# Kernel optimization log

Measured on AMD Instinct MI355X. Metric: run time of the kernel, lower is better.

The kernel has to match this reference:

```python
import jax, jax.numpy as jnp
import numpy as np

B, S, H, D = 4, 1024, 16, 128
E = H * D  # 2048
TOTAL = B * S
NUM_SLOTS = 2 * TOTAL


def setup_inputs() -> dict:
    key = jax.random.key(0)
    k1, k2, k3, k4, k5 = jax.random.split(key, 5)
    return {
        "hidden_states": jax.random.normal(k1, (TOTAL, E), dtype=jnp.float32) * 0.02,
        "c_attn_w": jax.random.normal(k2, (E, 3 * E), dtype=jnp.float32) * 0.02,
        "c_attn_b": jax.random.normal(k3, (3 * E,), dtype=jnp.float32) * 0.02,
        "c_proj_w": jax.random.normal(k4, (E, E), dtype=jnp.float32) * 0.02,
        "c_proj_b": jax.random.normal(k5, (E,), dtype=jnp.float32) * 0.02,
        "key_cache": jnp.zeros((NUM_SLOTS, H, D), dtype=jnp.float32),
        "value_cache": jnp.zeros((NUM_SLOTS, H, D), dtype=jnp.float32),
        "slots": jnp.arange(TOTAL, dtype=jnp.int32),
        "seq_len": S,
    }


def reference(hidden_states, c_attn_w, c_attn_b, c_proj_w, c_proj_b,
              key_cache, value_cache, slots, seq_len):
    total, embed = hidden_states.shape
    n_heads, head_dim = key_cache.shape[1], key_cache.shape[2]
    b = total // seq_len

    # fused QKV projection (fan_in_fan_out: y = x @ W + b)
    qkv = hidden_states @ c_attn_w + c_attn_b            # [total, 3E]
    qkv = qkv.reshape(total, 3, n_heads, head_dim)
    q, k, v = qkv[:, 0], qkv[:, 1], qkv[:, 2]

    # paged_attention.reshape_and_cache: scatter new k/v into the paged cache
    key_cache = key_cache.at[slots].set(k)
    value_cache = value_cache.at[slots].set(v)
    # prefill attention reads current tokens' k/v (gathered back from cache)
    k = key_cache[slots]
    v = value_cache[slots]

    # varlen causal flash attention over b equal-length sequences
    qb = q.reshape(b, seq_len, n_heads, head_dim)
    kb = k.reshape(b, seq_len, n_heads, head_dim)
    vb = v.reshape(b, seq_len, n_heads, head_dim)
    scale = jnp.asarray(head_dim, qb.dtype) ** -0.5       # softmax_scale
    scores = jnp.einsum("bqhd,bkhd->bhqk", qb, kb) * scale
    causal = jnp.tril(jnp.ones((seq_len, seq_len), dtype=bool))
    scores = jnp.where(causal, scores, jnp.finfo(scores.dtype).min)
    attn = jax.nn.softmax(scores, axis=-1)
    ctx = jnp.einsum("bhqk,bkhd->bqhd", attn, vb)
    ctx = ctx.reshape(total, embed)

    # output projection (fan_in_fan_out row-parallel linear)
    out = ctx @ c_proj_w + c_proj_b
    return out
```

## Files before the change

### kernel.cpp

```cpp
#include <hip/hip_runtime.h>
#include <stdint.h>

typedef __bf16 bf16x8 __attribute__((ext_vector_type(8)));
typedef float  f32x4  __attribute__((ext_vector_type(4)));

#define DEV static __device__ __forceinline__

DEV unsigned short f2bf(float x) {
    union { float f; unsigned int u; } v; v.f = x;
    unsigned int r = v.u + 0x7FFFu + ((v.u >> 16) & 1u);
    return (unsigned short)(r >> 16);
}

DEV unsigned short f2bf_hw(float x) {
    return __builtin_bit_cast(unsigned short, static_cast<__bf16>(x));
}

DEV void gl_lds16(const void* g, void* l) {
    __builtin_amdgcn_global_load_lds(
        (__attribute__((address_space(1))) void*)(g),
        (__attribute__((address_space(3))) void*)(l), 16, 0, 0);
}

DEV f32x4 zero4() { f32x4 z; z[0]=0.f; z[1]=0.f; z[2]=0.f; z[3]=0.f; return z; }

__global__ void k_prep(const float* __restrict__ hs, unsigned short* __restrict__ hs_bf,
                       const float* __restrict__ wqkv, unsigned short* __restrict__ wqkvT,
                       const float* __restrict__ wproj, unsigned short* __restrict__ wprojT) {
    __shared__ float tile[32][33];
    const int bid = blockIdx.x, t = threadIdx.x;
    if (bid < 2048) {
        #pragma unroll
        for (int j = 0; j < 4; j++) {
            int i = bid*4096 + j*1024 + t*4;
            float4 f = *(const float4*)(hs + i);
            ushort4 o;
            o.x = f2bf(f.x); o.y = f2bf(f.y); o.z = f2bf(f.z); o.w = f2bf(f.w);
            *(ushort4*)(hs_bf + i) = o;
        }
        return;
    }
    const float* in; unsigned short* out; int K, N, n0, k0;
    if (bid < 14336) {
        int ti = bid - 2048;
        in = wqkv; out = wqkvT; K = 2048; N = 6144;
        n0 = (ti % 192) * 32; k0 = (ti / 192) * 32;
    } else {
        int ti = bid - 14336;
        in = wproj; out = wprojT; K = 2048; N = 2048;
        n0 = (ti % 64) * 32; k0 = (ti / 64) * 32;
    }
    const int tr = t >> 3;
    const int tc = (t & 7) * 4;
    float4 f = *(const float4*)(in + (size_t)(k0 + tr) * N + n0 + tc);
    tile[tr][tc+0] = f.x; tile[tr][tc+1] = f.y; tile[tr][tc+2] = f.z; tile[tr][tc+3] = f.w;
    __syncthreads();
    ushort4 o;
    o.x = f2bf(tile[tc+0][tr]);
    o.y = f2bf(tile[tc+1][tr]);
    o.z = f2bf(tile[tc+2][tr]);
    o.w = f2bf(tile[tc+3][tr]);
    *(ushort4*)(out + (size_t)(n0 + tr) * K + k0 + tc) = o;
}

__launch_bounds__(256, 4)
__global__ void k_gemm_qkv(const unsigned short* __restrict__ A,
                           const unsigned short* __restrict__ BT,
                           const float* __restrict__ bias,
                           unsigned short* __restrict__ q_buf,
                           unsigned short* __restrict__ k_buf,
                           unsigned short* __restrict__ vt_buf,
                           int K) {
    __shared__ __align__(16) uint4 As[128*8];
    __shared__ __align__(16) uint4 Bs[128*8];

    const int t = threadIdx.x;
    const int wave = t >> 6, lane = t & 63, quad = lane >> 4, l15 = lane & 15;
    const int wm = wave & 1, wn = wave >> 1;
    const int bm = blockIdx.x, bn = blockIdx.y;

    f32x4 acc[4][4];
    #pragma unroll
    for (int i = 0; i < 4; i++)
        #pragma unroll
        for (int j = 0; j < 4; j++) acc[i][j] = zero4();

    int rS[4], gS[4];
    #pragma unroll
    for (int p = 0; p < 4; p++) {
        int c = p*4 + wave;
        int s = c*64 + lane;
        int r = s >> 3;
        rS[p] = r; gS[p] = (lane & 7) ^ (r & 7);
    }
    const unsigned short* Abase = A  + (size_t)(bm*128) * K;
    const unsigned short* Bbase = BT + (size_t)(bn*128) * K;

    const int kiters = K >> 6;
    for (int kk = 0; kk < kiters; kk++) {
        const int k0 = kk * 64;
        __syncthreads();
        #pragma unroll
        for (int p = 0; p < 4; p++) {
            int c = p*4 + wave;
            gl_lds16(Abase + (size_t)rS[p]*K + k0 + gS[p]*8, &As[c*64]);
            gl_lds16(Bbase + (size_t)rS[p]*K + k0 + gS[p]*8, &Bs[c*64]);
        }
        __syncthreads();
        #pragma unroll
        for (int ks = 0; ks < 2; ks++) {
            bf16x8 af[4], bfr[4];
            #pragma unroll
            for (int mt = 0; mt < 4; mt++) {
                int row = wm*64 + mt*16 + l15;
                int g = (ks*4 + quad) ^ (row & 7);
                af[mt] = __builtin_bit_cast(bf16x8, As[row*8 + g]);
            }
            #pragma unroll
            for (int nt = 0; nt < 4; nt++) {
                int row = wn*64 + nt*16 + l15;
                int g = (ks*4 + quad) ^ (row & 7);
                bfr[nt] = __builtin_bit_cast(bf16x8, Bs[row*8 + g]);
            }
            #pragma unroll
            for (int mt = 0; mt < 4; mt++)
                #pragma unroll
                for (int nt = 0; nt < 4; nt++)
                    acc[mt][nt] = __builtin_amdgcn_mfma_f32_16x16x32_bf16(
                        af[mt], bfr[nt], acc[mt][nt], 0, 0, 0);
        }
    }

    const int nglob = bn * 128;
    const int seg = nglob >> 11;
    const int cn_base = (nglob & 2047) + wn*64;
    if (seg < 2) {
        unsigned short* dst = (seg == 0) ? q_buf : k_buf;
        const float scl = (seg == 0) ? 0.12751743f : 1.0f;
        #pragma unroll
        for (int nt = 0; nt < 4; nt++) {
            int cn = cn_base + nt*16 + l15;
            float bv = bias[nglob + wn*64 + nt*16 + l15];
            #pragma unroll
            for (int mt = 0; mt < 4; mt++) {
                int tt = bm*128 + wm*64 + mt*16 + quad*4;
                #pragma unroll
                for (int r = 0; r < 4; r++)
                    dst[(size_t)(tt + r) * 2048 + cn] = f2bf((acc[mt][nt][r] + bv) * scl);
            }
        }
    } else {
        #pragma unroll
        for (int nt = 0; nt < 4; nt++) {
            int cn = cn_base + nt*16 + l15;
            int h = cn >> 7, d = cn & 127;
            float bv = bias[nglob + wn*64 + nt*16 + l15];
            #pragma unroll
            for (int mt = 0; mt < 4; mt++) {
                int tt = bm*128 + wm*64 + mt*16 + quad*4;
                int b = tt >> 10, s = tt & 1023;
                ushort4 pk;
                pk.x = f2bf(acc[mt][nt][0] + bv);
                pk.y = f2bf(acc[mt][nt][1] + bv);
                pk.z = f2bf(acc[mt][nt][2] + bv);
                pk.w = f2bf(acc[mt][nt][3] + bv);
                *(ushort4*)(vt_buf + ((size_t)((b*16 + h)*128 + d) * 1024 + s)) = pk;
            }
        }
    }
}

__launch_bounds__(256, 4)
__global__ void k_gemm_proj(const unsigned short* __restrict__ A,
                            const unsigned short* __restrict__ BT,
                            const float* __restrict__ bias,
                            float* __restrict__ outp,
                            int N, int K) {
    __shared__ __align__(16) uint4 As[128*8];
    __shared__ __align__(16) uint4 Bs[128*8];

    const int t = threadIdx.x;
    const int wave = t >> 6, lane = t & 63, quad = lane >> 4, l15 = lane & 15;
    const int wm = wave & 1, wn = wave >> 1;
    const int bm = blockIdx.x, bn = blockIdx.y;

    f32x4 acc[4][4];
    #pragma unroll
    for (int i = 0; i < 4; i++)
        #pragma unroll
        for (int j = 0; j < 4; j++) acc[i][j] = zero4();

    int rS[4], gS[4];
    #pragma unroll
    for (int p = 0; p < 4; p++) {
        int c = p*4 + wave;
        int s = c*64 + lane;
        int r = s >> 3;
        rS[p] = r; gS[p] = (lane & 7) ^ (r & 7);
    }
    const unsigned short* Abase = A  + (size_t)(bm*128) * K;
    const unsigned short* Bbase = BT + (size_t)(bn*128) * K;

    const int kiters = K >> 6;
    for (int kk = 0; kk < kiters; kk++) {
        const int k0 = kk * 64;
        __syncthreads();
        #pragma unroll
        for (int p = 0; p < 4; p++) {
            int c = p*4 + wave;
            gl_lds16(Abase + (size_t)rS[p]*K + k0 + gS[p]*8, &As[c*64]);
            gl_lds16(Bbase + (size_t)rS[p]*K + k0 + gS[p]*8, &Bs[c*64]);
        }
        __syncthreads();
        #pragma unroll
        for (int ks = 0; ks < 2; ks++) {
            bf16x8 af[4], bfr[4];
            #pragma unroll
            for (int mt = 0; mt < 4; mt++) {
                int row = wm*64 + mt*16 + l15;
                int g = (ks*4 + quad) ^ (row & 7);
                af[mt] = __builtin_bit_cast(bf16x8, As[row*8 + g]);
            }
            #pragma unroll
            for (int nt = 0; nt < 4; nt++) {
                int row = wn*64 + nt*16 + l15;
                int g = (ks*4 + quad) ^ (row & 7);
                bfr[nt] = __builtin_bit_cast(bf16x8, Bs[row*8 + g]);
            }
            #pragma unroll
            for (int mt = 0; mt < 4; mt++)
                #pragma unroll
                for (int nt = 0; nt < 4; nt++)
                    acc[mt][nt] = __builtin_amdgcn_mfma_f32_16x16x32_bf16(
                        af[mt], bfr[nt], acc[mt][nt], 0, 0, 0);
        }
    }

    #pragma unroll
    for (int nt = 0; nt < 4; nt++) {
        int n = bn*128 + wn*64 + nt*16 + l15;
        float bv = bias[n];
        #pragma unroll
        for (int mt = 0; mt < 4; mt++) {
            int m = bm*128 + wm*64 + mt*16 + quad*4;
            #pragma unroll
            for (int r = 0; r < 4; r++)
                outp[(size_t)(m + r) * N + n] = acc[mt][nt][r] + bv;
        }
    }
}

__launch_bounds__(256, 2)
__global__ void k_attn(const unsigned short* __restrict__ q_buf,
                       const unsigned short* __restrict__ k_buf,
                       const unsigned short* __restrict__ vt_buf,
                       unsigned short* __restrict__ ctx_buf) {
    extern __shared__ char smem[];
    uint4* Ks = (uint4*)smem;
    uint4* Vs = (uint4*)(smem + 32768);
    unsigned short* Pl = (unsigned short*)(smem + 65536);

    const int t = threadIdx.x;
    const int wave = t >> 6, lane = t & 63, quad = lane >> 4, l15 = lane & 15;
    const int bh = blockIdx.x;
    const int yq = blockIdx.y;
    const int qt = (yq < 4) ? yq : (11 - yq);
    const int b = bh >> 4, h = bh & 15;

    bf16x8 qf[2][4];
    #pragma unroll
    for (int rt = 0; rt < 2; rt++) {
        const size_t qoff = (size_t)(b*1024 + qt*128 + wave*32 + rt*16 + l15) * 2048 + h*128;
        #pragma unroll
        for (int ks = 0; ks < 4; ks++)
            qf[rt][ks] = __builtin_bit_cast(bf16x8, *(const uint4*)(q_buf + qoff + ks*32 + quad*8));
    }

    f32x4 ctx[2][8];
    #pragma unroll
    for (int rt = 0; rt < 2; rt++)
        #pragma unroll
        for (int i = 0; i < 8; i++) ctx[rt][i] = zero4();
    float l_run[2][4];
    #pragma unroll
    for (int rt = 0; rt < 2; rt++)
        #pragma unroll
        for (int r = 0; r < 4; r++) l_run[rt][r] = 0.f;

    const size_t kbase = (size_t)b * 1024 * 2048 + h*128;
    const size_t vbase = (size_t)(b*16 + h) * 131072;
    const int row0 = qt*128 + wave*32;
    const int kiters = 2*qt + 2;

    unsigned short* Plw = Pl + wave*1024;

    {
        #pragma unroll
        for (int p = 0; p < 4; p++) {
            int c = p*4 + wave;
            {   int s = c*64 + lane;
                int r = s >> 4;
                int g = (s & 15) ^ (r & 15);
                gl_lds16(k_buf + kbase + (size_t)(0*64 + r) * 2048 + g*8, Ks + c*64);
            }
            {   int s = c*64 + lane;
                int r = s >> 3;
                int g = (lane & 7) ^ (r & 7);
                gl_lds16(vt_buf + vbase + (size_t)r * 1024 + 0*64 + g*8, Vs + c*64);
            }
        }
    }
    __syncthreads();

    for (int kt = 0; kt < kiters; kt++) {
        const int d = kt & 1;

        if (kt + 1 < kiters) {
            const int dn = d ^ 1;
            #pragma unroll
            for (int p = 0; p < 4; p++) {
                int c = p*4 + wave;
                {   int s = c*64 + lane;
                    int r = s >> 4;
                    int g = (s & 15) ^ (r & 15);
                    gl_lds16(k_buf + kbase + (size_t)((kt+1)*64 + r) * 2048 + g*8,
                             Ks + dn*1024 + c*64);
                }
                {   int s = c*64 + lane;
                    int r = s >> 3;
                    int g = (lane & 7) ^ (r & 7);
                    gl_lds16(vt_buf + vbase + (size_t)r * 1024 + (kt+1)*64 + g*8,
                             Vs + dn*1024 + c*64);
                }
            }
        }

        if (kt*64 <= row0 + 31) {
            const bool needmask = (kt*64 + 63 > row0);
            const uint4* Kd = Ks + d*1024;
            const uint4* Vd = Vs + d*1024;

            f32x4 sacc[2][4];
            #pragma unroll
            for (int rt = 0; rt < 2; rt++)
                #pragma unroll
                for (int nt = 0; nt < 4; nt++) sacc[rt][nt] = zero4();
            #pragma unroll
            for (int ks = 0; ks < 4; ks++)
                #pragma unroll
                for (int nt = 0; nt < 4; nt++) {
                    int key = nt*16 + l15;
                    int g = (ks*4 + quad) ^ (key & 15);
                    bf16x8 kf = __builtin_bit_cast(bf16x8, Kd[key*16 + g]);
                    sacc[0][nt] = __builtin_amdgcn_mfma_f32_16x16x32_bf16(qf[0][ks], kf, sacc[0][nt], 0, 0, 0);
                    sacc[1][nt] = __builtin_amdgcn_mfma_f32_16x16x32_bf16(qf[1][ks], kf, sacc[1][nt], 0, 0, 0);
                }

            #pragma unroll
            for (int rt = 0; rt < 2; rt++) {
                float pv[4][4];
                if (needmask) {
                    #pragma unroll
                    for (int nt = 0; nt < 4; nt++)
                        #pragma unroll
                        for (int r = 0; r < 4; r++) {
                            bool masked = (kt*64 + nt*16 + l15 > row0 + rt*16 + quad*4 + r);
                            pv[nt][r] = masked ? 0.f : __builtin_amdgcn_exp2f(sacc[rt][nt][r]);
                        }
                } else {
                    #pragma unroll
                    for (int nt = 0; nt < 4; nt++)
                        #pragma unroll
                        for (int r = 0; r < 4; r++)
                            pv[nt][r] = __builtin_amdgcn_exp2f(sacc[rt][nt][r]);
                }
                #pragma unroll
                for (int r = 0; r < 4; r++)
                    l_run[rt][r] += (pv[0][r] + pv[1][r]) + (pv[2][r] + pv[3][r]);

                #pragma unroll
                for (int nt = 0; nt < 4; nt++)
                    #pragma unroll
                    for (int r = 0; r < 4; r++) {
                        int row = quad*4 + r;
                        int col = nt*16 + l15;
                        int gc = (col >> 3) ^ (row & 7);
                        Plw[row*64 + gc*8 + (col & 7)] = f2bf_hw(pv[nt][r]);
                    }
                __asm__ volatile("s_waitcnt lgkmcnt(0)" ::: "memory");

                #pragma unroll
                for (int ks = 0; ks < 2; ks++) {
                    int gp = (ks*4 + quad) ^ (l15 & 7);
                    bf16x8 pa = __builtin_bit_cast(bf16x8, *(const uint4*)&Plw[l15*64 + gp*8]);
                    #pragma unroll
                    for (int dt = 0; dt < 8; dt++) {
                        int drow = dt*16 + l15;
                        int gv = (ks*4 + quad) ^ (drow & 7);
                        bf16x8 vf = __builtin_bit_cast(bf16x8, Vd[drow*8 + gv]);
                        ctx[rt][dt] = __builtin_amdgcn_mfma_f32_16x16x32_bf16(pa, vf, ctx[rt][dt], 0, 0, 0);
                    }
                }
            }
        }

        __syncthreads();
    }

    #pragma unroll
    for (int rt = 0; rt < 2; rt++) {
        float inv[4];
        #pragma unroll
        for (int r = 0; r < 4; r++) {
            float l = l_run[rt][r];
            l += __shfl_xor(l, 1);
            l += __shfl_xor(l, 2);
            l += __shfl_xor(l, 4);
            l += __shfl_xor(l, 8);
            inv[r] = 1.0f / l;
        }
        const int tt0 = b*1024 + qt*128 + wave*32 + rt*16 + quad*4;
        #pragma unroll
        for (int dt = 0; dt < 8; dt++)
            #pragma unroll
            for (int r = 0; r < 4; r++)
                ctx_buf[(size_t)(tt0 + r) * 2048 + h*128 + dt*16 + l15] = f2bf_hw(ctx[rt][dt][r] * inv[r]);
    }
}

extern "C" void kernel_launch(void* const* d_in, const int* in_sizes, int n_in,
                              void* d_out, int out_size, void* d_ws, size_t ws_size,
                              hipStream_t stream) {
    const float* hs    = (const float*)d_in[0];
    const float* wqkv  = (const float*)d_in[1];
    const float* bqkv  = (const float*)d_in[2];
    const float* wproj = (const float*)d_in[3];
    const float* bproj = (const float*)d_in[4];

    char* ws = (char*)d_ws;
    unsigned short* hs_bf   = (unsigned short*)(ws);
    unsigned short* wqkvT   = (unsigned short*)(ws + 16777216ull);
    unsigned short* wprojT  = (unsigned short*)(ws + 41943040ull);
    unsigned short* q_buf   = (unsigned short*)(ws + 50331648ull);
    unsigned short* k_buf   = (unsigned short*)(ws + 67108864ull);
    unsigned short* vt_buf  = (unsigned short*)(ws + 83886080ull);
    unsigned short* ctx_buf = (unsigned short*)(ws + 100663296ull);

    static bool attr_set = false;
    if (!attr_set) {
        (void)hipFuncSetAttribute((const void*)k_attn,
                                  hipFuncAttributeMaxDynamicSharedMemorySize, 73728);
        attr_set = true;
    }

    k_prep<<<18432, 256, 0, stream>>>(hs, hs_bf, wqkv, wqkvT, wproj, wprojT);
    k_gemm_qkv<<<dim3(32, 48), 256, 0, stream>>>(hs_bf, wqkvT, bqkv, q_buf, k_buf, vt_buf, 2048);
    k_attn<<<dim3(64, 8), 256, 73728, stream>>>(q_buf, k_buf, vt_buf, ctx_buf);
    k_gemm_proj<<<dim3(32, 16), 256, 0, stream>>>(ctx_buf, wprojT, bproj, (float*)d_out, 2048, 2048);
}
```

Before: 381.8 us.

## Restructure QKV GEMM into 256x192 tiles with double-buffered LDS prefetch

Rewrites the QKV projection GEMM to use 512-thread workgroups computing 256x192 output tiles. The next K-slice is prefetched into a double-buffered dynamic LDS region while MFMAs run on the current one, with wave priority raised around the MFMA bursts. A swizzled block index improves L2 reuse across the 512 workgroups. The aim is to hide global-to-LDS latency and raise arithmetic intensity, at the cost of 112 KB LDS, one workgroup per CU, and higher register pressure.

```diff
diff --git a/kernel.cpp b/kernel.cpp
--- a/kernel.cpp
+++ b/kernel.cpp
@@ -63,101 +63,126 @@
     *(ushort4*)(out + (size_t)(n0 + tr) * K + k0 + tc) = o;
 }
 
-__launch_bounds__(256, 4)
+#define ST_A(NXT,K0,J) gl_lds16(Abase + (size_t)rA[J]*2048 + (K0) + gA[J], As + (NXT)*2048 + (J)*512 + dstw)
+#define ST_B(NXT,K0,J) gl_lds16(Bbase + (size_t)rB[J]*2048 + (K0) + gB[J], Bs + (NXT)*1536 + (J)*512 + dstw)
+
+#define QKV_TILE(CUR, NXT, TK)                                                  \
+  {                                                                             \
+    const uint4* Ar = As + (CUR)*2048;                                          \
+    const uint4* Br = Bs + (CUR)*1536;                                          \
+    const bool st = (TK) + 1 < 32;                                              \
+    const int kn = ((TK) + 1) * 64;                                             \
+    _Pragma("unroll")                                                           \
+    for (int p = 0; p < 4; ++p) {                                               \
+      const int mh = p >> 1, ks = p & 1;                                        \
+      bf16x8 af[4], bfr[3];                                                     \
+      _Pragma("unroll")                                                         \
+      for (int mt = 0; mt < 4; ++mt) {                                          \
+        int row = wm*128 + mh*64 + mt*16 + l15;                                 \
+        int g = (ks*4 + quad) ^ (row & 7);                                      \
+        af[mt] = __builtin_bit_cast(bf16x8, Ar[row*8 + g]);                     \
+      }                                                                         \
+      _Pragma("unroll")                                                         \
+      for (int nt = 0; nt < 3; ++nt) {                                          \
+        int row = wn*48 + nt*16 + l15;                                          \
+        int g = (ks*4 + quad) ^ (row & 7);                                      \
+        bfr[nt] = __builtin_bit_cast(bf16x8, Br[row*8 + g]);                    \
+      }                                                                         \
+      if (st && p == 0) { ST_A(NXT,kn,0); ST_A(NXT,kn,1); ST_A(NXT,kn,2); ST_A(NXT,kn,3); } \
+      if (st && p == 1) { ST_B(NXT,kn,0); ST_B(NXT,kn,1); ST_B(NXT,kn,2); }     \
+      __builtin_amdgcn_s_barrier();                                             \
+      __builtin_amdgcn_s_setprio(1);                                            \
+      _Pragma("unroll")                                                         \
+      for (int mt = 0; mt < 4; ++mt)                                            \
+        _Pragma("unroll")                                                       \
+        for (int nt = 0; nt < 3; ++nt)                                          \
+          acc[mh*4+mt][nt] = __builtin_amdgcn_mfma_f32_16x16x32_bf16(           \
+              af[mt], bfr[nt], acc[mh*4+mt][nt], 0, 0, 0);                      \
+      __builtin_amdgcn_s_setprio(0);                                            \
+      if (p < 3) __builtin_amdgcn_s_barrier();                                  \
+    }                                                                           \
+    if (st) {                                                                   \
+      asm volatile("s_waitcnt vmcnt(0)" ::: "memory");                          \
+      __builtin_amdgcn_s_barrier();                                             \
+      __builtin_amdgcn_sched_barrier(0);                                        \
+    }                                                                           \
+  }
+
+__launch_bounds__(512, 1)
 __global__ void k_gemm_qkv(const unsigned short* __restrict__ A,
                            const unsigned short* __restrict__ BT,
                            const float* __restrict__ bias,
                            unsigned short* __restrict__ q_buf,
                            unsigned short* __restrict__ k_buf,
-                           unsigned short* __restrict__ vt_buf,
-                           int K) {
-    __shared__ __align__(16) uint4 As[128*8];
-    __shared__ __align__(16) uint4 Bs[128*8];
+                           unsigned short* __restrict__ vt_buf) {
+    extern __shared__ char smem[];
+    uint4* As = (uint4*)smem;
+    uint4* Bs = (uint4*)(smem + 65536);
 
     const int t = threadIdx.x;
-    const int wave = t >> 6, lane = t & 63, quad = lane >> 4, l15 = lane & 15;
-    const int wm = wave & 1, wn = wave >> 1;
-    const int bm = blockIdx.x, bn = blockIdx.y;
-
-    f32x4 acc[4][4];
-    #pragma unroll
-    for (int i = 0; i < 4; i++)
-        #pragma unroll
-        for (int j = 0; j < 4; j++) acc[i][j] = zero4();
-
-    int rS[4], gS[4];
-    #pragma unroll
-    for (int p = 0; p < 4; p++) {
-        int c = p*4 + wave;
-        int s = c*64 + lane;
-        int r = s >> 3;
-        rS[p] = r; gS[p] = (lane & 7) ^ (r & 7);
-    }
-    const unsigned short* Abase = A  + (size_t)(bm*128) * K;
-    const unsigned short* Bbase = BT + (size_t)(bn*128) * K;
-
-    const int kiters = K >> 6;
-    for (int kk = 0; kk < kiters; kk++) {
-        const int k0 = kk * 64;
-        __syncthreads();
-        #pragma unroll
-        for (int p = 0; p < 4; p++) {
-            int c = p*4 + wave;
-            gl_lds16(Abase + (size_t)rS[p]*K + k0 + gS[p]*8, &As[c*64]);
-            gl_lds16(Bbase + (size_t)rS[p]*K + k0 + gS[p]*8, &Bs[c*64]);
-        }
-        __syncthreads();
-        #pragma unroll
-        for (int ks = 0; ks < 2; ks++) {
-            bf16x8 af[4], bfr[4];
-            #pragma unroll
-            for (int mt = 0; mt < 4; mt++) {
-                int row = wm*64 + mt*16 + l15;
-                int g = (ks*4 + quad) ^ (row & 7);
-                af[mt] = __builtin_bit_cast(bf16x8, As[row*8 + g]);
-            }
-            #pragma unroll
-            for (int nt = 0; nt < 4; nt++) {
-                int row = wn*64 + nt*16 + l15;
-                int g = (ks*4 + quad) ^ (row & 7);
-                bfr[nt] = __builtin_bit_cast(bf16x8, Bs[row*8 + g]);
-            }
-            #pragma unroll
-            for (int mt = 0; mt < 4; mt++)
-                #pragma unroll
-                for (int nt = 0; nt < 4; nt++)
-                    acc[mt][nt] = __builtin_amdgcn_mfma_f32_16x16x32_bf16(
-                        af[mt], bfr[nt], acc[mt][nt], 0, 0, 0);
-        }
-    }
-
-    const int nglob = bn * 128;
-    const int seg = nglob >> 11;
-    const int cn_base = (nglob & 2047) + wn*64;
-    if (seg < 2) {
-        unsigned short* dst = (seg == 0) ? q_buf : k_buf;
-        const float scl = (seg == 0) ? 0.12751743f : 1.0f;
-        #pragma unroll
-        for (int nt = 0; nt < 4; nt++) {
-            int cn = cn_base + nt*16 + l15;
-            float bv = bias[nglob + wn*64 + nt*16 + l15];
-            #pragma unroll
-            for (int mt = 0; mt < 4; mt++) {
-                int tt = bm*128 + wm*64 + mt*16 + quad*4;
+    const int wid = t >> 6, lane = t & 63, quad = lane >> 4, l15 = lane & 15;
+    const int wm = wid >> 2, wn = wid & 3;
+
+    const int wg = blockIdx.x;
+    const int swz = (wg & 7) * 64 + (wg >> 3);
+    const int bm = swz & 15, bn = swz >> 4;
+
+    f32x4 acc[8][3];
+    #pragma unroll
+    for (int i = 0; i < 8; i++)
+        #pragma unroll
+        for (int j = 0; j < 3; j++) acc[i][j] = zero4();
+
+    int rA[4], gA[4];
+    #pragma unroll
+    for (int j = 0; j < 4; j++) {
+        int s = j*512 + t, r = s >> 3;
+        rA[j] = r; gA[j] = ((s & 7) ^ (r & 7)) * 8;
+    }
+    int rB[3], gB[3];
+    #pragma unroll
+    for (int j = 0; j < 3; j++) {
+        int s = j*512 + t, r = s >> 3;
+        rB[j] = r; gB[j] = ((s & 7) ^ (r & 7)) * 8;
+    }
+    const unsigned short* Abase = A  + (size_t)(bm*256) * 2048;
+    const unsigned short* Bbase = BT + (size_t)(bn*192) * 2048;
+    const int dstw = wid * 64;
+
+    ST_A(0,0,0); ST_A(0,0,1); ST_A(0,0,2); ST_A(0,0,3);
+    ST_B(0,0,0); ST_B(0,0,1); ST_B(0,0,2);
+    asm volatile("s_waitcnt vmcnt(0)" ::: "memory");
+    __builtin_amdgcn_s_barrier();
+    __builtin_amdgcn_sched_barrier(0);
+
+    #pragma unroll 1
+    for (int j = 0; j < 16; ++j) {
+        QKV_TILE(0, 1, 2*j);
+        QKV_TILE(1, 0, 2*j + 1);
+    }
+
+    const int nbase = bn*192 + wn*48;
+    #pragma unroll
+    for (int nt = 0; nt < 3; nt++) {
+        const int cn = nbase + nt*16 + l15;
+        const int seg = cn >> 11;
+        const int cv = cn & 2047;
+        const float bv = bias[cn];
+        if (seg < 2) {
+            unsigned short* dst = (seg == 0) ? q_buf : k_buf;
+            const float scl = (seg == 0) ? 0.12751743f : 1.0f;
+            #pragma unroll
+            for (int mt = 0; mt < 8; mt++) {
+                int tt = bm*256 + wm*128 + mt*16 + quad*4;
                 #pragma unroll
                 for (int r = 0; r < 4; r++)
-                    dst[(size_t)(tt + r) * 2048 + cn] = f2bf((acc[mt][nt][r] + bv) * scl);
-            }
-        }
-    } else {
-        #pragma unroll
-        for (int nt = 0; nt < 4; nt++) {
-            int cn = cn_base + nt*16 + l15;
-            int h = cn >> 7, d = cn & 127;
-            float bv = bias[nglob + wn*64 + nt*16 + l15];
-            #pragma unroll
-            for (int mt = 0; mt < 4; mt++) {
-                int tt = bm*128 + wm*64 + mt*16 + quad*4;
+                    dst[(size_t)(tt + r) * 2048 + cv] = f2bf((acc[mt][nt][r] + bv) * scl);
+            }
+        } else {
+            const int h = cv >> 7, d = cv & 127;
+            #pragma unroll
+            for (int mt = 0; mt < 8; mt++) {
+                int tt = bm*256 + wm*128 + mt*16 + quad*4;
                 int b = tt >> 10, s = tt & 1023;
                 ushort4 pk;
                 pk.x = f2bf(acc[mt][nt][0] + bv);
@@ -169,6 +194,9 @@
         }
     }
 }
+#undef QKV_TILE
+#undef ST_A
+#undef ST_B
 
 __launch_bounds__(256, 4)
 __global__ void k_gemm_proj(const unsigned short* __restrict__ A,
@@ -450,11 +478,13 @@
     if (!attr_set) {
         (void)hipFuncSetAttribute((const void*)k_attn,
                                   hipFuncAttributeMaxDynamicSharedMemorySize, 73728);
+        (void)hipFuncSetAttribute((const void*)k_gemm_qkv,
+                                  hipFuncAttributeMaxDynamicSharedMemorySize, 114688);
         attr_set = true;
     }
 
     k_prep<<<18432, 256, 0, stream>>>(hs, hs_bf, wqkv, wqkvT, wproj, wprojT);
-    k_gemm_qkv<<<dim3(32, 48), 256, 0, stream>>>(hs_bf, wqkvT, bqkv, q_buf, k_buf, vt_buf, 2048);
+    k_gemm_qkv<<<512, 512, 114688, stream>>>(hs_bf, wqkvT, bqkv, q_buf, k_buf, vt_buf);
     k_attn<<<dim3(64, 8), 256, 73728, stream>>>(q_buf, k_buf, vt_buf, ctx_buf);
     k_gemm_proj<<<dim3(32, 16), 256, 0, stream>>>(ctx_buf, wprojT, bproj, (float*)d_out, 2048, 2048);
 }
```

Result: slower. 394.5 us (+3.3%).
